# Kernel optimization log

Measured on AMD Instinct MI355X. Metric: run time of the kernel, lower is better.

Reference implementation:

```python
import jax, jax.numpy as jnp
import numpy as np

B, T = 1048576, 8
ALPHA = 1.1
COMMISSION = 0.05
BET_PCT = 0.02  # assumed bet_percentage (undefined in original __init__)
TAU = 0.1
EPS = 1e-8


def setup_inputs() -> dict:
    key = jax.random.key(0)
    k1, k2, k3, k4 = jax.random.split(key, 4)
    # network outputs are probabilities (used as probs in entropy/profit terms)
    predicted_probs = jax.nn.softmax(jax.random.normal(k1, (B, T), dtype=jnp.float32), axis=1)
    # one-hot true winners
    winner_idx = jax.random.randint(k2, (B,), 0, T)
    true_winners = jax.nn.one_hot(winner_idx, T, dtype=jnp.float32)
    # decimal odds in [1.5, 15): valid and complete field for nearly all races
    market_odds = jax.random.uniform(k3, (B, T), dtype=jnp.float32, minval=1.5, maxval=15.0)
    # explicit Gumbel(0,1) noise standing in for F.gumbel_softmax's internal sample
    u = jax.random.uniform(k4, (B, T), dtype=jnp.float32, minval=1e-6, maxval=1.0 - 1e-6)
    gumbel_noise = -jnp.log(-jnp.log(u))
    return {"predicted_probs": predicted_probs, "true_winners": true_winners,
            "market_odds": market_odds, "gumbel_noise": gumbel_noise}


def reference(predicted_probs, true_winners, market_odds, gumbel_noise):
    batch_size = predicted_probs.shape[0]
    # race validity
    has_valid_odds = jnp.any(market_odds > 0, axis=1)
    implied_probs = 1.0 / jnp.clip(market_odds, 1.01)
    has_complete_field = implied_probs.sum(axis=1) >= 0.95
    valid = has_valid_odds & has_complete_field  # [B]

    # masked expected profit per dog
    ep = jnp.where(valid[:, None],
                   (market_odds * ALPHA * predicted_probs - 1.0) * BET_PCT * (1.0 - COMMISSION),
                   0.0)  # [B,T]

    # gumbel-softmax selection (logits = ep / temperature, tau = temperature)
    soft_selection = jax.nn.softmax((ep / TAU + gumbel_noise) / TAU, axis=1)
    soft_expected_profits = (soft_selection * ep).sum(axis=1)  # [B]

    # prediction cross-entropy (probs treated as logits, per original code)
    labels = jnp.argmax(true_winners, axis=1)
    logp = jax.nn.log_softmax(predicted_probs, axis=1)
    ce = -jnp.take_along_axis(logp, labels[:, None], axis=1)[:, 0]  # [B]

    valid_f = valid.astype(ce.dtype)
    cnt = valid_f.sum()
    prediction_loss = jnp.where(cnt > 0, (ce * valid_f).sum() / jnp.maximum(cnt, 1.0), ce.mean())

    confidence_penalty = -predicted_probs.max(axis=1).mean() * 0.1
    betting_loss = jnp.where(cnt > 0, -(soft_expected_profits * valid_f).sum() / batch_size,
                             confidence_penalty)

    entropy_reg = -(predicted_probs * jnp.log(predicted_probs + EPS)).sum(axis=1).mean()

    lambda_betting = jnp.minimum(0.5 + cnt / 10000.0 * 0.5, 1.0)
    lambda_entropy = 0.01
    loss = prediction_loss + lambda_betting * betting_loss - lambda_entropy * entropy_reg
    return loss
```

## Files before the change

### kernel.cpp

```cpp
#include <hip/hip_runtime.h>
#include <math.h>


constexpr int T = 8;
constexpr int NB = 1024;
constexpr int NT = 256;

__global__ __launch_bounds__(NT) void betting_main(
    const float* __restrict__ pp, const float* __restrict__ tw,
    const float* __restrict__ mo, const float* __restrict__ gn,
    float* __restrict__ partials, int nraces) {
  int tid = blockIdx.x * blockDim.x + threadIdx.x;
  int stride = gridDim.x * blockDim.x;

  float acc[6] = {0.f, 0.f, 0.f, 0.f, 0.f, 0.f};

  for (int r = tid; r < nraces; r += stride) {
    const float4* pp4 = (const float4*)pp;
    const float4* tw4 = (const float4*)tw;
    const float4* mo4 = (const float4*)mo;
    const float4* gn4 = (const float4*)gn;
    float4 a0 = pp4[r * 2], a1 = pp4[r * 2 + 1];
    float4 b0 = tw4[r * 2], b1 = tw4[r * 2 + 1];
    float4 c0 = mo4[r * 2], c1 = mo4[r * 2 + 1];
    float4 d0 = gn4[r * 2], d1 = gn4[r * 2 + 1];

    float p[T] = {a0.x, a0.y, a0.z, a0.w, a1.x, a1.y, a1.z, a1.w};
    float w[T] = {b0.x, b0.y, b0.z, b0.w, b1.x, b1.y, b1.z, b1.w};
    float o[T] = {c0.x, c0.y, c0.z, c0.w, c1.x, c1.y, c1.z, c1.w};
    float g[T] = {d0.x, d0.y, d0.z, d0.w, d1.x, d1.y, d1.z, d1.w};

    bool anypos = false;
    float simp = 0.f;
#pragma unroll
    for (int t = 0; t < T; ++t) {
      anypos = anypos || (o[t] > 0.f);
      simp += 1.f / fmaxf(o[t], 1.01f);
    }
    bool valid = anypos && (simp >= 0.95f);
    float vf = valid ? 1.f : 0.f;

    float ep[T];
#pragma unroll
    for (int t = 0; t < T; ++t)
      ep[t] = valid ? (o[t] * 1.1f * p[t] - 1.f) * (0.02f * 0.95f) : 0.f;

    float z[T], zm = -INFINITY;
#pragma unroll
    for (int t = 0; t < T; ++t) {
      z[t] = ep[t] * 100.f + g[t] * 10.f;
      zm = fmaxf(zm, z[t]);
    }
    float s2 = 0.f, sp = 0.f;
#pragma unroll
    for (int t = 0; t < T; ++t) {
      float e = __expf(z[t] - zm);
      s2 += e;
      sp += e * ep[t];
    }
    float soft_ep = sp / s2;

    float m = -INFINITY;
#pragma unroll
    for (int t = 0; t < T; ++t) m = fmaxf(m, p[t]);
    float se = 0.f, plabel = 0.f;
#pragma unroll
    for (int t = 0; t < T; ++t) {
      se += __expf(p[t] - m);
      plabel += w[t] * p[t];
    }
    float ce = m + __logf(se) - plabel;

    float ent = 0.f;
#pragma unroll
    for (int t = 0; t < T; ++t) ent -= p[t] * __logf(p[t] + 1e-8f);

    acc[0] += vf;
    acc[1] += ce * vf;
    acc[2] += ce;
    acc[3] += soft_ep * vf;
    acc[4] += m;
    acc[5] += ent;
  }

  __shared__ float red[NT / 64][6];
#pragma unroll
  for (int k = 0; k < 6; ++k) {
#pragma unroll
    for (int off = 32; off >= 1; off >>= 1) acc[k] += __shfl_down(acc[k], off);
  }
  int lane = threadIdx.x & 63, wave = threadIdx.x >> 6;
  if (lane == 0) {
#pragma unroll
    for (int k = 0; k < 6; ++k) red[wave][k] = acc[k];
  }
  __syncthreads();
  if (threadIdx.x == 0) {
#pragma unroll
    for (int k = 0; k < 6; ++k) {
      float s = 0.f;
      for (int wv = 0; wv < NT / 64; ++wv) s += red[wv][k];
      partials[k * gridDim.x + blockIdx.x] = s;
    }
  }
}

__global__ __launch_bounds__(NT) void betting_final(
    const float* __restrict__ partials, int nb, float* __restrict__ out,
    double Bd) {
  __shared__ double red[NT / 64][6];
  double a[6] = {0, 0, 0, 0, 0, 0};
#pragma unroll
  for (int k = 0; k < 6; ++k)
    for (int i = threadIdx.x; i < nb; i += NT) a[k] += (double)partials[k * nb + i];
#pragma unroll
  for (int k = 0; k < 6; ++k) {
#pragma unroll
    for (int off = 32; off >= 1; off >>= 1) a[k] += __shfl_down(a[k], off);
  }
  int lane = threadIdx.x & 63, wave = threadIdx.x >> 6;
  if (lane == 0) {
#pragma unroll
    for (int k = 0; k < 6; ++k) red[wave][k] = a[k];
  }
  __syncthreads();
  if (threadIdx.x == 0) {
    double s[6];
#pragma unroll
    for (int k = 0; k < 6; ++k) {
      s[k] = 0.0;
      for (int wv = 0; wv < NT / 64; ++wv) s[k] += red[wv][k];
    }
    double cnt = s[0], Scev = s[1], Sce = s[2], Ssoft = s[3], Smax = s[4],
           Sent = s[5];
    double pred = (cnt > 0.0) ? Scev / fmax(cnt, 1.0) : Sce / Bd;
    double conf = -(Smax / Bd) * 0.1;
    double bet = (cnt > 0.0) ? -Ssoft / Bd : conf;
    double ent = Sent / Bd;
    double lam = fmin(0.5 + cnt / 10000.0 * 0.5, 1.0);
    out[0] = (float)(pred + lam * bet - 0.01 * ent);
  }
}

extern "C" void kernel_launch(void* const* d_in, const int* in_sizes, int n_in,
                              void* d_out, int out_size, void* d_ws,
                              size_t ws_size, hipStream_t stream) {
  const float* pp = (const float*)d_in[0];
  const float* tw = (const float*)d_in[1];
  const float* mo = (const float*)d_in[2];
  const float* gn = (const float*)d_in[3];
  float* out = (float*)d_out;
  float* partials = (float*)d_ws;

  int nraces = in_sizes[0] / T;

  betting_main<<<NB, NT, 0, stream>>>(pp, tw, mo, gn, partials, nraces);
  betting_final<<<1, NT, 0, stream>>>(partials, NB, out, (double)nraces);
}
```

Measured before the change: 36.00 us.

## Split each race across two lanes for coalesced float4 loads with shuffle reductions

Each race is now handled by two adjacent lanes, each loading one float4 per input, so a wavefront's loads are fully contiguous instead of strided by 32 bytes. The per-race max and sum reductions are finished with xor shuffles between the lane pair, and the accumulated terms are halved so the totals stay the same. The grid grows to up to 4096 blocks, capped by workspace size, and the reciprocals use the hardware rcp approximation. The cost is extra shuffle instructions and more partials for the final kernel to reduce.

```diff
diff --git a/kernel.cpp b/kernel.cpp
--- a/kernel.cpp
+++ b/kernel.cpp
@@ -2,85 +2,85 @@
 #include <math.h>
 
 
-constexpr int T = 8;
-constexpr int NB = 1024;
 constexpr int NT = 256;
 
-__global__ __launch_bounds__(NT) void betting_main(
-    const float* __restrict__ pp, const float* __restrict__ tw,
-    const float* __restrict__ mo, const float* __restrict__ gn,
-    float* __restrict__ partials, int nraces) {
-  int tid = blockIdx.x * blockDim.x + threadIdx.x;
-  int stride = gridDim.x * blockDim.x;
+__device__ __forceinline__ float fastrcp(float x) {
+  return __builtin_amdgcn_rcpf(x);
+}
+
+__global__ __launch_bounds__(NT, 4) void betting_main(
+    const float4* __restrict__ pp4, const float4* __restrict__ tw4,
+    const float4* __restrict__ mo4, const float4* __restrict__ gn4,
+    float* __restrict__ partials, int nhalf) {
+  const int tid = blockIdx.x * NT + threadIdx.x;
+  const int ntot = gridDim.x * NT;
 
   float acc[6] = {0.f, 0.f, 0.f, 0.f, 0.f, 0.f};
 
-  for (int r = tid; r < nraces; r += stride) {
-    const float4* pp4 = (const float4*)pp;
-    const float4* tw4 = (const float4*)tw;
-    const float4* mo4 = (const float4*)mo;
-    const float4* gn4 = (const float4*)gn;
-    float4 a0 = pp4[r * 2], a1 = pp4[r * 2 + 1];
-    float4 b0 = tw4[r * 2], b1 = tw4[r * 2 + 1];
-    float4 c0 = mo4[r * 2], c1 = mo4[r * 2 + 1];
-    float4 d0 = gn4[r * 2], d1 = gn4[r * 2 + 1];
+  for (int f = tid; f < nhalf; f += ntot) {
+    float4 av = pp4[f];
+    float4 wv = tw4[f];
+    float4 ov = mo4[f];
+    float4 gv = gn4[f];
+    float p[4] = {av.x, av.y, av.z, av.w};
+    float w[4] = {wv.x, wv.y, wv.z, wv.w};
+    float o[4] = {ov.x, ov.y, ov.z, ov.w};
+    float g[4] = {gv.x, gv.y, gv.z, gv.w};
 
-    float p[T] = {a0.x, a0.y, a0.z, a0.w, a1.x, a1.y, a1.z, a1.w};
-    float w[T] = {b0.x, b0.y, b0.z, b0.w, b1.x, b1.y, b1.z, b1.w};
-    float o[T] = {c0.x, c0.y, c0.z, c0.w, c1.x, c1.y, c1.z, c1.w};
-    float g[T] = {d0.x, d0.y, d0.z, d0.w, d1.x, d1.y, d1.z, d1.w};
+    float anyp = 0.f, simp = 0.f;
+#pragma unroll
+    for (int t = 0; t < 4; ++t) {
+      anyp = fmaxf(anyp, (o[t] > 0.f) ? 1.f : 0.f);
+      simp += fastrcp(fmaxf(o[t], 1.01f));
+    }
+    anyp = fmaxf(anyp, __shfl_xor(anyp, 1));
+    simp = simp + __shfl_xor(simp, 1);
+    float vf = (anyp > 0.5f && simp >= 0.95f) ? 1.f : 0.f;
 
-    bool anypos = false;
-    float simp = 0.f;
+    float ep[4];
 #pragma unroll
-    for (int t = 0; t < T; ++t) {
-      anypos = anypos || (o[t] > 0.f);
-      simp += 1.f / fmaxf(o[t], 1.01f);
+    for (int t = 0; t < 4; ++t)
+      ep[t] = (o[t] * 1.1f * p[t] - 1.f) * (0.02f * 0.95f) * vf;
+
+    float z[4], zmh = -INFINITY;
+#pragma unroll
+    for (int t = 0; t < 4; ++t) {
+      z[t] = ep[t] * 100.f + g[t] * 10.f;
+      zmh = fmaxf(zmh, z[t]);
     }
-    bool valid = anypos && (simp >= 0.95f);
-    float vf = valid ? 1.f : 0.f;
+    float zm = fmaxf(zmh, __shfl_xor(zmh, 1));
+    float s2h = 0.f, sph = 0.f;
+#pragma unroll
+    for (int t = 0; t < 4; ++t) {
+      float e = __expf(z[t] - zm);
+      s2h += e;
+      sph += e * ep[t];
+    }
+    float s2 = s2h + __shfl_xor(s2h, 1);
+    float sp = sph + __shfl_xor(sph, 1);
+    float soft_ep = sp * fastrcp(s2);
 
-    float ep[T];
+    float mh = fmaxf(fmaxf(p[0], p[1]), fmaxf(p[2], p[3]));
+    float m = fmaxf(mh, __shfl_xor(mh, 1));
+    float seh = 0.f, plh = 0.f;
 #pragma unroll
-    for (int t = 0; t < T; ++t)
-      ep[t] = valid ? (o[t] * 1.1f * p[t] - 1.f) * (0.02f * 0.95f) : 0.f;
+    for (int t = 0; t < 4; ++t) {
+      seh += __expf(p[t] - m);
+      plh += w[t] * p[t];
+    }
+    float se = seh + __shfl_xor(seh, 1);
+    float celin = 0.5f * (m + __logf(se)) - plh;
 
-    float z[T], zm = -INFINITY;
+    float enth = 0.f;
 #pragma unroll
-    for (int t = 0; t < T; ++t) {
-      z[t] = ep[t] * 100.f + g[t] * 10.f;
-      zm = fmaxf(zm, z[t]);
-    }
-    float s2 = 0.f, sp = 0.f;
-#pragma unroll
-    for (int t = 0; t < T; ++t) {
-      float e = __expf(z[t] - zm);
-      s2 += e;
-      sp += e * ep[t];
-    }
-    float soft_ep = sp / s2;
+    for (int t = 0; t < 4; ++t) enth -= p[t] * __logf(p[t] + 1e-8f);
 
-    float m = -INFINITY;
-#pragma unroll
-    for (int t = 0; t < T; ++t) m = fmaxf(m, p[t]);
-    float se = 0.f, plabel = 0.f;
-#pragma unroll
-    for (int t = 0; t < T; ++t) {
-      se += __expf(p[t] - m);
-      plabel += w[t] * p[t];
-    }
-    float ce = m + __logf(se) - plabel;
-
-    float ent = 0.f;
-#pragma unroll
-    for (int t = 0; t < T; ++t) ent -= p[t] * __logf(p[t] + 1e-8f);
-
-    acc[0] += vf;
-    acc[1] += ce * vf;
-    acc[2] += ce;
-    acc[3] += soft_ep * vf;
-    acc[4] += m;
-    acc[5] += ent;
+    acc[0] += 0.5f * vf;
+    acc[1] += celin * vf;
+    acc[2] += celin;
+    acc[3] += 0.5f * soft_ep * vf;
+    acc[4] += 0.5f * m;
+    acc[5] += enth;
   }
 
   __shared__ float red[NT / 64][6];
@@ -145,15 +145,19 @@
 extern "C" void kernel_launch(void* const* d_in, const int* in_sizes, int n_in,
                               void* d_out, int out_size, void* d_ws,
                               size_t ws_size, hipStream_t stream) {
-  const float* pp = (const float*)d_in[0];
-  const float* tw = (const float*)d_in[1];
-  const float* mo = (const float*)d_in[2];
-  const float* gn = (const float*)d_in[3];
+  const float4* pp = (const float4*)d_in[0];
+  const float4* tw = (const float4*)d_in[1];
+  const float4* mo = (const float4*)d_in[2];
+  const float4* gn = (const float4*)d_in[3];
   float* out = (float*)d_out;
   float* partials = (float*)d_ws;
 
-  int nraces = in_sizes[0] / T;
+  int nraces = in_sizes[0] / 8;
+  int nhalf = nraces * 2;
 
-  betting_main<<<NB, NT, 0, stream>>>(pp, tw, mo, gn, partials, nraces);
-  betting_final<<<1, NT, 0, stream>>>(partials, NB, out, (double)nraces);
+  int nb = 4096;
+  while ((size_t)(6 * nb * 4) > ws_size && nb > 64) nb >>= 1;
+
+  betting_main<<<nb, NT, 0, stream>>>(pp, tw, mo, gn, partials, nhalf);
+  betting_final<<<1, NT, 0, stream>>>(partials, nb, out, (double)nraces);
 }
```

New measurement: 51.98 us. 44.4% more time.
